# Kernel optimization log

Hardware: AMD Instinct MI355X
Metric: run time of the kernel (lower is better)

The kernel has to match this reference:

```python
import jax, jax.numpy as jnp
import numpy as np

D = 16777216  # d_in

def spu(t):
    # SPU activation: x^2 - 0.5 for x >= 0, sigmoid(-x) - 1 for x < 0
    return jnp.where(t >= 0, t * t - 0.5, jax.nn.sigmoid(-t) - 1.0)

def dx_spu(t):
    sig = jax.nn.sigmoid(-t)
    return jnp.where(t >= 0, 2.0 * t, -sig * (1.0 - sig))


def setup_inputs() -> dict:
    key = jax.random.key(0)
    kx, kl, ku = jax.random.split(key, 3)
    x = jax.random.normal(kx, (D, 1), dtype=jnp.float32)
    # valid interval l < x < u with strict margin
    l_in = x - jax.random.uniform(kl, (D, 1), dtype=jnp.float32, minval=1e-3, maxval=2.0)
    u_in = x + jax.random.uniform(ku, (D, 1), dtype=jnp.float32, minval=1e-3, maxval=2.0)
    return {"x": x, "l_in": l_in, "u_in": u_in}


def _bounds(x, l, u):
    # heuristic 'x': p_l = x, then clamped to [l, u]
    p = jnp.clip(x, l, u)
    spu_l, spu_u, spu_p = spu(l), spu(u), spu(p)

    # chord through (l, spu(l)) and (u, spu(u))  (l < u guaranteed)
    chord_slope = (spu_u - spu_l) / (u - l)
    chord_int = spu_l - chord_slope * l

    # tangent at p
    tan_slope = dx_spu(p)
    tan_int = spu_p - p * tan_slope

    # line through (l, spu(l)) and (0, spu(0) = -0.5); only used when u>0, p<0 => l<0
    safe_l = jnp.where(l != 0, l, 1.0)
    l0_slope = (-0.5 - spu_l) / (0.0 - safe_l)
    l0_int = -0.5  # intercept at x=0

    u_pos = u > 0
    p_nonneg = p >= 0

    # u > 0: ub = chord; lb = tangent at p if p>=0 else line (l,spu(l))-(0,-0.5)
    # u <= 0: lb = chord; ub = tangent at p
    lb_slope = jnp.where(u_pos, jnp.where(p_nonneg, tan_slope, l0_slope), chord_slope)
    lb_int = jnp.where(u_pos, jnp.where(p_nonneg, tan_int, l0_int), chord_int)
    ub_slope = jnp.where(u_pos, chord_slope, tan_slope)
    ub_int = jnp.where(u_pos, chord_int, tan_int)

    # faithful reproduction of the original output formulas (including the
    # lb_slope term inside u_out's else-branch, as written in the source)
    l_out = lb_int + jnp.where(lb_slope > 0, l * (-lb_slope), u * lb_slope)
    u_out = ub_int + jnp.where(ub_slope > 0, u * ub_slope, l * (-lb_slope))
    return l_out, u_out


def reference(x, l_in, u_in):
    x_out = spu(x)
    l_out, u_out = _bounds(x, l_in, u_in)
    return (x_out, l_out, u_out)
```

## Files before the change

### kernel.cpp

```cpp
#include <hip/hip_runtime.h>


__device__ __forceinline__ float sig_negt(float t) {
    return 1.0f / (1.0f + __expf(t));
}

__device__ __forceinline__ float spu_f(float t) {
    float s = sig_negt(t);
    return (t >= 0.0f) ? (t * t - 0.5f) : (s - 1.0f);
}

__device__ __forceinline__ float dx_spu_f(float t) {
    float s = sig_negt(t);
    return (t >= 0.0f) ? (2.0f * t) : (-s * (1.0f - s));
}

__device__ __forceinline__ void spu_elem(float x, float l, float u,
                                         float& x_out, float& l_out, float& u_out) {
    x_out = spu_f(x);

    float p = fminf(fmaxf(x, l), u);

    float spu_l = spu_f(l);
    float spu_u = spu_f(u);
    float spu_p = spu_f(p);

    float chord_slope = (spu_u - spu_l) / (u - l);
    float chord_int   = spu_l - chord_slope * l;

    float tan_slope = dx_spu_f(p);
    float tan_int   = spu_p - p * tan_slope;

    float safe_l   = (l != 0.0f) ? l : 1.0f;
    float l0_slope = (-0.5f - spu_l) / (0.0f - safe_l);
    float l0_int   = -0.5f;

    bool u_pos    = (u > 0.0f);
    bool p_nonneg = (p >= 0.0f);

    float lb_slope = u_pos ? (p_nonneg ? tan_slope : l0_slope) : chord_slope;
    float lb_int   = u_pos ? (p_nonneg ? tan_int   : l0_int)   : chord_int;
    float ub_slope = u_pos ? chord_slope : tan_slope;
    float ub_int   = u_pos ? chord_int   : tan_int;

    l_out = lb_int + ((lb_slope > 0.0f) ? (l * (-lb_slope)) : (u * lb_slope));
    u_out = ub_int + ((ub_slope > 0.0f) ? (u * ub_slope)    : (l * (-lb_slope)));
}

__global__ void __launch_bounds__(256)
spu_transformer_kernel(const float4* __restrict__ x,
                       const float4* __restrict__ l,
                       const float4* __restrict__ u,
                       float4* __restrict__ out_x,
                       float4* __restrict__ out_l,
                       float4* __restrict__ out_u,
                       int n4) {
    int stride = gridDim.x * blockDim.x;
    for (int i = blockIdx.x * blockDim.x + threadIdx.x; i < n4; i += stride) {
        float4 xv = x[i];
        float4 lv = l[i];
        float4 uv = u[i];
        float4 ox, ol, ou;
        spu_elem(xv.x, lv.x, uv.x, ox.x, ol.x, ou.x);
        spu_elem(xv.y, lv.y, uv.y, ox.y, ol.y, ou.y);
        spu_elem(xv.z, lv.z, uv.z, ox.z, ol.z, ou.z);
        spu_elem(xv.w, lv.w, uv.w, ox.w, ol.w, ou.w);
        out_x[i] = ox;
        out_l[i] = ol;
        out_u[i] = ou;
    }
}

extern "C" void kernel_launch(void* const* d_in, const int* in_sizes, int n_in,
                              void* d_out, int out_size, void* d_ws, size_t ws_size,
                              hipStream_t stream) {
    const float* x = (const float*)d_in[0];
    const float* l = (const float*)d_in[1];
    const float* u = (const float*)d_in[2];
    float* out = (float*)d_out;

    const int D  = in_sizes[0];
    const int n4 = D / 4;

    float* out_x = out;
    float* out_l = out + D;
    float* out_u = out + 2 * (size_t)D;

    const int block = 256;
    int grid = 2048;
    int max_grid = (n4 + block - 1) / block;
    if (grid > max_grid) grid = max_grid;

    spu_transformer_kernel<<<grid, block, 0, stream>>>(
        (const float4*)x, (const float4*)l, (const float4*)u,
        (float4*)out_x, (float4*)out_l, (float4*)out_u, n4);
}
```

Before: 339.9 us.

## Use nontemporal vector loads/stores, one-shot grid, and hardware reciprocal

Replaces the grid-stride loop with one float4 per thread over a full-size grid, and switches global loads and stores to nontemporal builtins so the streaming data bypasses cache retention. Divisions are replaced by the hardware approximate reciprocal. This aims to cut memory-path overhead and divide cost in a bandwidth-bound elementwise kernel, at the cost of slightly lower precision and far more launched blocks.

```diff
diff --git a/kernel.cpp b/kernel.cpp
--- a/kernel.cpp
+++ b/kernel.cpp
@@ -1,8 +1,14 @@
 #include <hip/hip_runtime.h>
 
 
+typedef float float4n __attribute__((ext_vector_type(4)));
+
+__device__ __forceinline__ float fast_rcp(float a) {
+    return __builtin_amdgcn_rcpf(a);
+}
+
 __device__ __forceinline__ float sig_negt(float t) {
-    return 1.0f / (1.0f + __expf(t));
+    return fast_rcp(1.0f + __expf(t));
 }
 
 __device__ __forceinline__ float spu_f(float t) {
@@ -25,14 +31,14 @@
     float spu_u = spu_f(u);
     float spu_p = spu_f(p);
 
-    float chord_slope = (spu_u - spu_l) / (u - l);
+    float chord_slope = (spu_u - spu_l) * fast_rcp(u - l);
     float chord_int   = spu_l - chord_slope * l;
 
     float tan_slope = dx_spu_f(p);
     float tan_int   = spu_p - p * tan_slope;
 
     float safe_l   = (l != 0.0f) ? l : 1.0f;
-    float l0_slope = (-0.5f - spu_l) / (0.0f - safe_l);
+    float l0_slope = (-0.5f - spu_l) * fast_rcp(-safe_l);
     float l0_int   = -0.5f;
 
     bool u_pos    = (u > 0.0f);
@@ -48,27 +54,34 @@
 }
 
 __global__ void __launch_bounds__(256)
-spu_transformer_kernel(const float4* __restrict__ x,
-                       const float4* __restrict__ l,
-                       const float4* __restrict__ u,
-                       float4* __restrict__ out_x,
-                       float4* __restrict__ out_l,
-                       float4* __restrict__ out_u,
+spu_transformer_kernel(const float4n* __restrict__ x,
+                       const float4n* __restrict__ l,
+                       const float4n* __restrict__ u,
+                       float4n* __restrict__ out_x,
+                       float4n* __restrict__ out_l,
+                       float4n* __restrict__ out_u,
                        int n4) {
-    int stride = gridDim.x * blockDim.x;
-    for (int i = blockIdx.x * blockDim.x + threadIdx.x; i < n4; i += stride) {
-        float4 xv = x[i];
-        float4 lv = l[i];
-        float4 uv = u[i];
-        float4 ox, ol, ou;
-        spu_elem(xv.x, lv.x, uv.x, ox.x, ol.x, ou.x);
-        spu_elem(xv.y, lv.y, uv.y, ox.y, ol.y, ou.y);
-        spu_elem(xv.z, lv.z, uv.z, ox.z, ol.z, ou.z);
-        spu_elem(xv.w, lv.w, uv.w, ox.w, ol.w, ou.w);
-        out_x[i] = ox;
-        out_l[i] = ol;
-        out_u[i] = ou;
-    }
+    int i = blockIdx.x * blockDim.x + threadIdx.x;
+    if (i >= n4) return;
+
+    float4n xv = __builtin_nontemporal_load(&x[i]);
+    float4n lv = __builtin_nontemporal_load(&l[i]);
+    float4n uv = __builtin_nontemporal_load(&u[i]);
+
+    float oxa[4], ola[4], oua[4];
+    spu_elem(xv.x, lv.x, uv.x, oxa[0], ola[0], oua[0]);
+    spu_elem(xv.y, lv.y, uv.y, oxa[1], ola[1], oua[1]);
+    spu_elem(xv.z, lv.z, uv.z, oxa[2], ola[2], oua[2]);
+    spu_elem(xv.w, lv.w, uv.w, oxa[3], ola[3], oua[3]);
+
+    float4n ox, ol, ou;
+    ox.x = oxa[0]; ox.y = oxa[1]; ox.z = oxa[2]; ox.w = oxa[3];
+    ol.x = ola[0]; ol.y = ola[1]; ol.z = ola[2]; ol.w = ola[3];
+    ou.x = oua[0]; ou.y = oua[1]; ou.z = oua[2]; ou.w = oua[3];
+
+    __builtin_nontemporal_store(ox, &out_x[i]);
+    __builtin_nontemporal_store(ol, &out_l[i]);
+    __builtin_nontemporal_store(ou, &out_u[i]);
 }
 
 extern "C" void kernel_launch(void* const* d_in, const int* in_sizes, int n_in,
@@ -83,15 +96,13 @@
     const int n4 = D / 4;
 
     float* out_x = out;
-    float* out_l = out + D;
+    float* out_l = out + (size_t)D;
     float* out_u = out + 2 * (size_t)D;
 
     const int block = 256;
-    int grid = 2048;
-    int max_grid = (n4 + block - 1) / block;
-    if (grid > max_grid) grid = max_grid;
+    const int grid  = (n4 + block - 1) / block;
 
     spu_transformer_kernel<<<grid, block, 0, stream>>>(
-        (const float4*)x, (const float4*)l, (const float4*)u,
-        (float4*)out_x, (float4*)out_l, (float4*)out_u, n4);
+        (const float4n*)x, (const float4n*)l, (const float4n*)u,
+        (float4n*)out_x, (float4n*)out_l, (float4n*)out_u, n4);
 }
```

Result: faster. 319.0 us (-6.2%).
